# Performance work log

Hardware: AMD Instinct MI355X
Metric: run time of the kernel (lower is better)

The kernel has to match this reference:

```python
import jax, jax.numpy as jnp
import numpy as np

N = 100000   # nodes
E = 1600000  # edges (avg degree 16)
F_IN = 50    # dataset.num_features
C = 32       # dataset.num_classes == hidden == out channels


def setup_inputs() -> dict:
    key = jax.random.key(0)
    ks = jax.random.split(key, 12)
    x = jax.random.normal(ks[0], (N, F_IN), dtype=jnp.float32)
    edge_index = jax.random.randint(ks[1], (2, E), 0, N, dtype=jnp.int64)
    dims = [(F_IN, C), (C, C), (C, C)]
    inp = {"x": x, "edge_index": edge_index}
    for i, (din, dout) in enumerate(dims, start=1):
        s = 1.0 / np.sqrt(din)
        inp[f"Wl{i}"] = jax.random.uniform(ks[2 + 3 * (i - 1)], (din, dout), jnp.float32, -s, s)
        inp[f"bl{i}"] = jax.random.uniform(ks[3 + 3 * (i - 1)], (dout,), jnp.float32, -s, s)
        inp[f"Wr{i}"] = jax.random.uniform(ks[4 + 3 * (i - 1)], (din, dout), jnp.float32, -s, s)
    return inp


def _sage_conv(x, src, dst, Wl, bl, Wr):
    # message = x[src]; scatter-max into dst; lin_l(agg) + lin_r(x)
    msg = x[src]                                      # [E, d_in]
    agg = jax.ops.segment_max(msg, dst, num_segments=N)
    agg = jnp.where(jnp.isfinite(agg), agg, jnp.zeros((), agg.dtype))  # empty segments -> 0
    return agg @ Wl + bl + x @ Wr


def reference(x, edge_index, Wl1, bl1, Wr1, Wl2, bl2, Wr2, Wl3, bl3, Wr3):
    src, dst = edge_index[0], edge_index[1]
    h = jax.nn.relu(_sage_conv(x, src, dst, Wl1, bl1, Wr1))
    h = jax.nn.relu(_sage_conv(h, src, dst, Wl2, bl2, Wr2))
    h = _sage_conv(h, src, dst, Wl3, bl3, Wr3)
    return jax.nn.log_softmax(h, axis=1)
```

## Files before the change

kernel.cpp:

```cpp
#include <hip/hip_runtime.h>
#include <math.h>

#define NN 100000
#define CD 32
#define NPB 4

#define B1N ((NN + 255) >> 8)
#define EPB_A 4096

typedef unsigned int   uint32;
typedef unsigned short ushort16;

__device__ __forceinline__ ushort16 f2b(float f) {
    uint32 u = __float_as_uint(f);
    u = (u + 0x7FFFu + ((u >> 16) & 1u)) >> 16;
    return (ushort16)u;
}
__device__ __forceinline__ float b2f_lo(uint32 u) { return __uint_as_float(u << 16); }
__device__ __forceinline__ float b2f_hi(uint32 u) { return __uint_as_float(u & 0xFFFF0000u); }

__global__ void detect_idx64(const void* edge, int* flag) {
    const long long* p = (const long long*)edge;
    int lane = threadIdx.x & 63;
    int bad = 0;
    for (int i = lane; i < 512; i += 64) {
        long long v = p[i];
        if (v < 0 || v >= NN) bad = 1;
    }
    unsigned long long anybad = __ballot(bad);
    if (lane == 0) *flag = (anybad == 0ULL) ? 1 : 0;
}

__device__ __forceinline__ int load_idx(const void* edge, int i, int is64) {
    if (is64) return (int)((const long long*)edge)[i];
    return ((const int*)edge)[i];
}

__global__ void cvt_x_kernel(const float* __restrict__ x, uint32* __restrict__ xb) {
    const int t = blockIdx.x * blockDim.x + threadIdx.x;
    if (t >= NN * 32) return;
    const int n = t >> 5;
    const int c = t & 31;
    if (c >= 25) { xb[t] = 0; return; }
    float2 v = *(const float2*)&x[n * 50 + 2 * c];
    xb[t] = (uint32)f2b(v.x) | ((uint32)f2b(v.y) << 16);
}


__global__ __launch_bounds__(256) void hist_kernel(const void* edge, int E,
                                                   const int* flag,
                                                   int* __restrict__ hist) {
    __shared__ int lh[B1N];
    const int is64 = *flag;
    const int t = threadIdx.x;
    for (int b = t; b < B1N; b += 256) lh[b] = 0;
    __syncthreads();
    const int e0 = blockIdx.x * EPB_A + t;
#pragma unroll
    for (int k = 0; k < 16; ++k) {
        int e = e0 + k * 256;
        if (e < E) {
            int d = load_idx(edge, E + e, is64);
            atomicAdd(&lh[d >> 8], 1);
        }
    }
    __syncthreads();
    int* gh = hist + (size_t)blockIdx.x * B1N;
    for (int b = t; b < B1N; b += 256) gh[b] = lh[b];
}

__global__ __launch_bounds__(256) void scanA_kernel(int* __restrict__ hist,
                                                    int nblk,
                                                    int* __restrict__ binTotal) {
    __shared__ int ts[256];
    const int bin = blockIdx.x;
    const int t = threadIdx.x;
    const int base = t * 4;
    int v0 = (base + 0 < nblk) ? hist[(size_t)(base + 0) * B1N + bin] : 0;
    int v1 = (base + 1 < nblk) ? hist[(size_t)(base + 1) * B1N + bin] : 0;
    int v2 = (base + 2 < nblk) ? hist[(size_t)(base + 2) * B1N + bin] : 0;
    int v3 = (base + 3 < nblk) ? hist[(size_t)(base + 3) * B1N + bin] : 0;
    const int s = v0 + v1 + v2 + v3;
    ts[t] = s;
    __syncthreads();
    for (int off = 1; off < 256; off <<= 1) {
        int u = (t >= off) ? ts[t - off] : 0;
        __syncthreads();
        ts[t] += u;
        __syncthreads();
    }
    int e = ts[t] - s;
    if (base + 0 < nblk) { hist[(size_t)(base + 0) * B1N + bin] = e; e += v0; }
    if (base + 1 < nblk) { hist[(size_t)(base + 1) * B1N + bin] = e; e += v1; }
    if (base + 2 < nblk) { hist[(size_t)(base + 2) * B1N + bin] = e; e += v2; }
    if (base + 3 < nblk) { hist[(size_t)(base + 3) * B1N + bin] = e; e += v3; }
    if (t == 255) binTotal[bin] = ts[255];
}

__global__ __launch_bounds__(256) void scanB_kernel(const int* __restrict__ binTotal,
                                                    int* __restrict__ binBase) {
    __shared__ int ts[256];
    const int t = threadIdx.x;
    const int base = t * 2;
    const int v0 = (base + 0 < B1N) ? binTotal[base + 0] : 0;
    const int v1 = (base + 1 < B1N) ? binTotal[base + 1] : 0;
    const int s = v0 + v1;
    ts[t] = s;
    __syncthreads();
    for (int off = 1; off < 256; off <<= 1) {
        int u = (t >= off) ? ts[t - off] : 0;
        __syncthreads();
        ts[t] += u;
        __syncthreads();
    }
    const int e = ts[t] - s;
    if (base + 0 < B1N) binBase[base + 0] = e;
    if (base + 1 < B1N) binBase[base + 1] = e + v0;
    if (t == 255) binBase[B1N] = ts[255];
}

__global__ __launch_bounds__(256) void scatter_kernel(const void* edge, int E,
                                                      const int* flag,
                                                      const int* __restrict__ hist,
                                                      const int* __restrict__ binBase,
                                                      uint32* __restrict__ bucketed) {
    __shared__ int cur[B1N];
    const int is64 = *flag;
    const int t = threadIdx.x;
    const int* gh = hist + (size_t)blockIdx.x * B1N;
    for (int b = t; b < B1N; b += 256) cur[b] = binBase[b] + gh[b];
    __syncthreads();
    const int e0 = blockIdx.x * EPB_A + t;
#pragma unroll
    for (int k = 0; k < 16; ++k) {
        int e = e0 + k * 256;
        if (e < E) {
            int s = load_idx(edge, e, is64);
            int d = load_idx(edge, E + e, is64);
            int pos = atomicAdd(&cur[d >> 8], 1);
            bucketed[pos] = (uint32)s | ((uint32)(d & 255) << 17);
        }
    }
}

__global__ __launch_bounds__(256) void bucket_kernel(const uint32* __restrict__ bucketed,
                                                     const int* __restrict__ binBase,
                                                     int* __restrict__ offsets,
                                                     int* __restrict__ csr_src) {
    __shared__ int h[256];
    __shared__ int sc[256];
    __shared__ int cur[256];
    const int bkt = blockIdx.x;
    const int t = threadIdx.x;
    const int start = binBase[bkt];
    const int end   = binBase[bkt + 1];
    h[t] = 0;
    __syncthreads();
    for (int i = start + t; i < end; i += 256)
        atomicAdd(&h[bucketed[i] >> 17], 1);
    __syncthreads();
    const int v = h[t];
    sc[t] = v;
    __syncthreads();
    for (int off = 1; off < 256; off <<= 1) {
        int u = (t >= off) ? sc[t - off] : 0;
        __syncthreads();
        sc[t] += u;
        __syncthreads();
    }
    const int excl = sc[t] - v;
    const int node = bkt * 256 + t;
    if (node < NN) offsets[node] = start + excl;
    cur[t] = start + excl;
    __syncthreads();
    for (int i = start + t; i < end; i += 256) {
        uint32 p = bucketed[i];
        int pos = atomicAdd(&cur[p >> 17], 1);
        csr_src[pos] = (int)(p & 0x1FFFFu);
    }
    if (bkt == B1N - 1 && t == 0) offsets[NN] = end;
}

__global__ void gather50_kernel(const uint32* __restrict__ hb,
                                const int* __restrict__ offsets,
                                const int* __restrict__ csr_src,
                                uint32* __restrict__ aggB) {
    const int tid  = threadIdx.x;
    const int g    = tid >> 6;
    const int lane = tid & 63;
    const int p    = lane >> 5;
    const int j    = lane & 31;
    const int n    = blockIdx.x * NPB + g;
    if (n >= NN) return;

    const float NEG = -INFINITY;
    const int beg = offsets[n];
    const int end = offsets[n + 1];
    const char* hbase = (const char*)hb;
    const uint32 joff = (uint32)(j << 2);

    float lo_[8], hi_[8];
#pragma unroll
    for (int k = 0; k < 8; ++k) { lo_[k] = NEG; hi_[k] = NEG; }
    int i = beg + p;
    for (; i + 14 < end; i += 16) {
        int s[8];
#pragma unroll
        for (int k = 0; k < 8; ++k) s[k] = csr_src[i + 2 * k];
#pragma unroll
        for (int k = 0; k < 8; ++k) {
            uint32 u = *(const uint32*)(hbase + ((((uint32)s[k]) << 7) | joff));
            lo_[k] = fmaxf(lo_[k], b2f_lo(u));
            hi_[k] = fmaxf(hi_[k], b2f_hi(u));
        }
    }
#pragma unroll
    for (int k = 0; k < 7; ++k) {
        if (i + 2 * k < end) {
            uint32 u = *(const uint32*)(hbase + ((((uint32)csr_src[i + 2 * k]) << 7) | joff));
            lo_[k] = fmaxf(lo_[k], b2f_lo(u));
            hi_[k] = fmaxf(hi_[k], b2f_hi(u));
        }
    }
#pragma unroll
    for (int off2 = 4; off2 > 0; off2 >>= 1)
#pragma unroll
        for (int k = 0; k < off2; ++k) {
            lo_[k] = fmaxf(lo_[k], lo_[k + off2]);
            hi_[k] = fmaxf(hi_[k], hi_[k + off2]);
        }
    float lo = lo_[0], hi = hi_[0];
    lo = fmaxf(lo, __shfl_xor(lo, 32));
    hi = fmaxf(hi, __shfl_xor(hi, 32));
    lo = (lo == NEG) ? 0.0f : lo;
    hi = (hi == NEG) ? 0.0f : hi;
    if (p == 0 && j < 25) {
        aggB[(size_t)n * 32 + j] =
            (__float_as_uint(lo) >> 16) | (__float_as_uint(hi) & 0xFFFF0000u);
    }
}

__global__ void gather32_kernel(const uint32* __restrict__ hb,
                                const int* __restrict__ offsets,
                                const int* __restrict__ csr_src,
                                uint32* __restrict__ aggB) {
    const int tid  = threadIdx.x;
    const int g    = tid >> 6;
    const int lane = tid & 63;
    const int e    = lane >> 4;
    const int c    = lane & 15;
    const int n    = blockIdx.x * NPB + g;
    if (n >= NN) return;

    const float NEG = -INFINITY;
    const int beg = offsets[n];
    const int end = offsets[n + 1];
    const char* hbase = (const char*)hb;
    const uint32 coff = (uint32)(c << 2);

    float l0 = NEG, h0 = NEG, l1 = NEG, h1 = NEG;
    float l2 = NEG, h2 = NEG, l3 = NEG, h3 = NEG;
    int i = beg + e;
    for (; i + 12 < end; i += 16) {
        int s0 = csr_src[i];
        int s1 = csr_src[i + 4];
        int s2 = csr_src[i + 8];
        int s3 = csr_src[i + 12];
        uint32 u0 = *(const uint32*)(hbase + ((((uint32)s0) << 6) | coff));
        uint32 u1 = *(const uint32*)(hbase + ((((uint32)s1) << 6) | coff));
        uint32 u2 = *(const uint32*)(hbase + ((((uint32)s2) << 6) | coff));
        uint32 u3 = *(const uint32*)(hbase + ((((uint32)s3) << 6) | coff));
        l0 = fmaxf(l0, b2f_lo(u0)); h0 = fmaxf(h0, b2f_hi(u0));
        l1 = fmaxf(l1, b2f_lo(u1)); h1 = fmaxf(h1, b2f_hi(u1));
        l2 = fmaxf(l2, b2f_lo(u2)); h2 = fmaxf(h2, b2f_hi(u2));
        l3 = fmaxf(l3, b2f_lo(u3)); h3 = fmaxf(h3, b2f_hi(u3));
    }
    if (i < end) {
        uint32 u = *(const uint32*)(hbase + ((((uint32)csr_src[i]) << 6) | coff));
        l0 = fmaxf(l0, b2f_lo(u)); h0 = fmaxf(h0, b2f_hi(u));
    }
    if (i + 4 < end) {
        uint32 u = *(const uint32*)(hbase + ((((uint32)csr_src[i + 4]) << 6) | coff));
        l1 = fmaxf(l1, b2f_lo(u)); h1 = fmaxf(h1, b2f_hi(u));
    }
    if (i + 8 < end) {
        uint32 u = *(const uint32*)(hbase + ((((uint32)csr_src[i + 8]) << 6) | coff));
        l2 = fmaxf(l2, b2f_lo(u)); h2 = fmaxf(h2, b2f_hi(u));
    }
    float lo = fmaxf(fmaxf(l0, l1), fmaxf(l2, l3));
    float hi = fmaxf(fmaxf(h0, h1), fmaxf(h2, h3));
    lo = fmaxf(lo, __shfl_xor(lo, 16));
    hi = fmaxf(hi, __shfl_xor(hi, 16));
    lo = fmaxf(lo, __shfl_xor(lo, 32));
    hi = fmaxf(hi, __shfl_xor(hi, 32));
    lo = (lo == NEG) ? 0.0f : lo;
    hi = (hi == NEG) ? 0.0f : hi;
    if (lane < 16) {
        aggB[(size_t)n * 16 + lane] =
            (__float_as_uint(lo) >> 16) | (__float_as_uint(hi) & 0xFFFF0000u);
    }
}

template <int DIN, int ASTR, int HSTR, int OSTR, int MODE>
__global__ void dense_kernel(const uint32* __restrict__ aggB,
                             const uint32* __restrict__ hB,
                             const float* __restrict__ Wl,
                             const float* __restrict__ bl,
                             const float* __restrict__ Wr,
                             void* __restrict__ out_v) {
    const int n = blockIdx.x * blockDim.x + threadIdx.x;
    if (n >= NN) return;

    float acc[CD];
#pragma unroll
    for (int j = 0; j < CD; ++j) acc[j] = bl[j];

    {
        const uint32* row = aggB + (size_t)n * ASTR;
        for (int c = 0; c < DIN / 4; ++c) {
            uint2 u = *(const uint2*)&row[c * 2];
            float d0 = b2f_lo(u.x), d1 = b2f_hi(u.x);
            float d2 = b2f_lo(u.y), d3 = b2f_hi(u.y);
            const float* w = Wl + c * 4 * CD;
#pragma unroll
            for (int j = 0; j < CD; ++j)
                acc[j] += d0 * w[j] + d1 * w[CD + j] + d2 * w[2 * CD + j] + d3 * w[3 * CD + j];
        }
        if (DIN % 4) {
            uint32 u = row[(DIN / 4) * 2];
            float d0 = b2f_lo(u), d1 = b2f_hi(u);
            const float* w = Wl + (DIN - 2) * CD;
#pragma unroll
            for (int j = 0; j < CD; ++j)
                acc[j] += d0 * w[j] + d1 * w[CD + j];
        }
    }
    {
        const uint32* row = hB + (size_t)n * HSTR;
        for (int c = 0; c < DIN / 4; ++c) {
            uint2 u = *(const uint2*)&row[c * 2];
            float d0 = b2f_lo(u.x), d1 = b2f_hi(u.x);
            float d2 = b2f_lo(u.y), d3 = b2f_hi(u.y);
            const float* w = Wr + c * 4 * CD;
#pragma unroll
            for (int j = 0; j < CD; ++j)
                acc[j] += d0 * w[j] + d1 * w[CD + j] + d2 * w[2 * CD + j] + d3 * w[3 * CD + j];
        }
        if (DIN % 4) {
            uint32 u = row[(DIN / 4) * 2];
            float d0 = b2f_lo(u), d1 = b2f_hi(u);
            const float* w = Wr + (DIN - 2) * CD;
#pragma unroll
            for (int j = 0; j < CD; ++j)
                acc[j] += d0 * w[j] + d1 * w[CD + j];
        }
    }

    if (MODE == 0) {
        uint32* orow = (uint32*)out_v + (size_t)n * OSTR;
#pragma unroll
        for (int c = 0; c < CD / 2; ++c) {
            float a0 = fmaxf(acc[2 * c],     0.0f);
            float a1 = fmaxf(acc[2 * c + 1], 0.0f);
            orow[c] = (uint32)f2b(a0) | ((uint32)f2b(a1) << 16);
        }
    } else {
        float m = acc[0];
#pragma unroll
        for (int j = 1; j < CD; ++j) m = fmaxf(m, acc[j]);
        float s = 0.0f;
#pragma unroll
        for (int j = 0; j < CD; ++j) s += expf(acc[j] - m);
        const float lse = m + logf(s);
        float* orow = (float*)out_v + (size_t)n * CD;
#pragma unroll
        for (int j = 0; j < CD; ++j) orow[j] = acc[j] - lse;
    }
}

extern "C" void kernel_launch(void* const* d_in, const int* in_sizes, int n_in,
                              void* d_out, int out_size, void* d_ws, size_t ws_size,
                              hipStream_t stream) {
    const float* x    = (const float*)d_in[0];
    const void*  edge = d_in[1];
    const float* Wl1 = (const float*)d_in[2];
    const float* bl1 = (const float*)d_in[3];
    const float* Wr1 = (const float*)d_in[4];
    const float* Wl2 = (const float*)d_in[5];
    const float* bl2 = (const float*)d_in[6];
    const float* Wr2 = (const float*)d_in[7];
    const float* Wl3 = (const float*)d_in[8];
    const float* bl3 = (const float*)d_in[9];
    const float* Wr3 = (const float*)d_in[10];

    const int E = in_sizes[1] / 2;

    char* ws = (char*)d_ws;
    size_t off = 0;
    auto carve = [&](size_t bytes) {
        void* p = ws + off;
        off = (off + bytes + 255) & ~(size_t)255;
        return p;
    };
    int*    offsets   = (int*)   carve((size_t)(NN + 1) * 4);
    int*    flag      = (int*)   carve(4);
    int*    binTotal  = (int*)   carve((size_t)B1N * 4);
    int*    binBase   = (int*)   carve((size_t)(B1N + 1) * 4);
    int*    csr_src   = (int*)   carve((size_t)E * 4);
    uint32* xb        = (uint32*)carve((size_t)NN * 32 * 4);
    uint32* h1b       = (uint32*)carve((size_t)NN * 16 * 4);
    (void)ws_size; (void)n_in; (void)out_size;

    uint32* bucketed = (uint32*)d_out;
    int*    hist     = (int*)((char*)d_out + (((size_t)E * 4 + 255) & ~(size_t)255));
    uint32* agg1 = (uint32*)d_out;
    uint32* agg2 = (uint32*)d_out;
    uint32* h2b  = xb;
    uint32* agg3 = h1b;

    detect_idx64<<<1, 64, 0, stream>>>(edge, flag);
    cvt_x_kernel<<<(NN * 32 + 255) / 256, 256, 0, stream>>>(x, xb);

    const int nblkA = (E + EPB_A - 1) / EPB_A;
    hist_kernel<<<nblkA, 256, 0, stream>>>(edge, E, flag, hist);
    scanA_kernel<<<B1N, 256, 0, stream>>>(hist, nblkA, binTotal);
    scanB_kernel<<<1, 256, 0, stream>>>(binTotal, binBase);
    scatter_kernel<<<nblkA, 256, 0, stream>>>(edge, E, flag, hist, binBase, bucketed);
    bucket_kernel<<<B1N, 256, 0, stream>>>(bucketed, binBase, offsets, csr_src);

    const int gb = (NN + NPB - 1) / NPB;
    const int db = (NN + 255) / 256;

    gather50_kernel<<<gb, 256, 0, stream>>>(xb, offsets, csr_src, agg1);
    dense_kernel<50, 32, 32, 16, 0><<<db, 256, 0, stream>>>(agg1, xb, Wl1, bl1, Wr1, h1b);
    gather32_kernel<<<gb, 256, 0, stream>>>(h1b, offsets, csr_src, agg2);
    dense_kernel<32, 16, 16, 16, 0><<<db, 256, 0, stream>>>(agg2, h1b, Wl2, bl2, Wr2, h2b);
    gather32_kernel<<<gb, 256, 0, stream>>>(h2b, offsets, csr_src, agg3);
    dense_kernel<32, 16, 16, 0, 2><<<db, 256, 0, stream>>>(agg3, h2b, Wl3, bl3, Wr3, d_out);
}
```

Before: 344.0 us.

## Fuse gather and dense phases per layer; inline index-width detect and bin scan

Merges each layer's neighbor max-gather with its dense projection into one kernel. The aggregate and self features stay in LDS and each wavefront computes the 32 outputs with lanes split across the Wl and Wr halves, so the bf16 aggregate no longer round-trips through global memory. The index-width detection kernel and the single-block bin-base scan are folded into their consumer kernels, where every block recomputes them redundantly, and edges per block are halved. This removes several launches and intermediate buffers, at the cost of per-lane serial dot products reading weights from global or cache and repeated small scans in each block.

After: 342.1 us. No clear change (-0.6%).

```diff
diff --git a/kernel.cpp b/kernel.cpp
--- a/kernel.cpp
+++ b/kernel.cpp
@@ -6,7 +6,7 @@
 #define NPB 4
 
 #define B1N ((NN + 255) >> 8)
-#define EPB_A 4096
+#define EPB_A 2048
 
 typedef unsigned int   uint32;
 typedef unsigned short ushort16;
@@ -19,7 +19,7 @@
 __device__ __forceinline__ float b2f_lo(uint32 u) { return __uint_as_float(u << 16); }
 __device__ __forceinline__ float b2f_hi(uint32 u) { return __uint_as_float(u & 0xFFFF0000u); }
 
-__global__ void detect_idx64(const void* edge, int* flag) {
+__device__ __forceinline__ int edge_is64(const void* edge) {
     const long long* p = (const long long*)edge;
     int lane = threadIdx.x & 63;
     int bad = 0;
@@ -28,7 +28,7 @@
         if (v < 0 || v >= NN) bad = 1;
     }
     unsigned long long anybad = __ballot(bad);
-    if (lane == 0) *flag = (anybad == 0ULL) ? 1 : 0;
+    return (anybad == 0ULL) ? 1 : 0;
 }
 
 __device__ __forceinline__ int load_idx(const void* edge, int i, int is64) {
@@ -48,16 +48,15 @@
 
 
 __global__ __launch_bounds__(256) void hist_kernel(const void* edge, int E,
-                                                   const int* flag,
                                                    int* __restrict__ hist) {
     __shared__ int lh[B1N];
-    const int is64 = *flag;
+    const int is64 = edge_is64(edge);
     const int t = threadIdx.x;
     for (int b = t; b < B1N; b += 256) lh[b] = 0;
     __syncthreads();
     const int e0 = blockIdx.x * EPB_A + t;
 #pragma unroll
-    for (int k = 0; k < 16; ++k) {
+    for (int k = 0; k < 8; ++k) {
         int e = e0 + k * 256;
         if (e < E) {
             int d = load_idx(edge, E + e, is64);
@@ -97,9 +96,8 @@
     if (t == 255) binTotal[bin] = ts[255];
 }
 
-__global__ __launch_bounds__(256) void scanB_kernel(const int* __restrict__ binTotal,
-                                                    int* __restrict__ binBase) {
-    __shared__ int ts[256];
+__device__ __forceinline__ void scan_bins_lds(const int* __restrict__ binTotal,
+                                              int* ts, int* lbase) {
     const int t = threadIdx.x;
     const int base = t * 2;
     const int v0 = (base + 0 < B1N) ? binTotal[base + 0] : 0;
@@ -114,25 +112,28 @@
         __syncthreads();
     }
     const int e = ts[t] - s;
-    if (base + 0 < B1N) binBase[base + 0] = e;
-    if (base + 1 < B1N) binBase[base + 1] = e + v0;
-    if (t == 255) binBase[B1N] = ts[255];
+    if (base + 0 < B1N) lbase[base + 0] = e;
+    if (base + 1 < B1N) lbase[base + 1] = e + v0;
+    if (t == 255) lbase[B1N] = ts[255];
+    __syncthreads();
 }
 
 __global__ __launch_bounds__(256) void scatter_kernel(const void* edge, int E,
-                                                      const int* flag,
                                                       const int* __restrict__ hist,
-                                                      const int* __restrict__ binBase,
+                                                      const int* __restrict__ binTotal,
                                                       uint32* __restrict__ bucketed) {
+    __shared__ int ts[256];
+    __shared__ int lbase[B1N + 1];
     __shared__ int cur[B1N];
-    const int is64 = *flag;
+    const int is64 = edge_is64(edge);
     const int t = threadIdx.x;
+    scan_bins_lds(binTotal, ts, lbase);
     const int* gh = hist + (size_t)blockIdx.x * B1N;
-    for (int b = t; b < B1N; b += 256) cur[b] = binBase[b] + gh[b];
+    for (int b = t; b < B1N; b += 256) cur[b] = lbase[b] + gh[b];
     __syncthreads();
     const int e0 = blockIdx.x * EPB_A + t;
 #pragma unroll
-    for (int k = 0; k < 16; ++k) {
+    for (int k = 0; k < 8; ++k) {
         int e = e0 + k * 256;
         if (e < E) {
             int s = load_idx(edge, e, is64);
@@ -144,16 +145,19 @@
 }
 
 __global__ __launch_bounds__(256) void bucket_kernel(const uint32* __restrict__ bucketed,
-                                                     const int* __restrict__ binBase,
+                                                     const int* __restrict__ binTotal,
                                                      int* __restrict__ offsets,
                                                      int* __restrict__ csr_src) {
+    __shared__ int ts[256];
+    __shared__ int lbase[B1N + 1];
     __shared__ int h[256];
     __shared__ int sc[256];
     __shared__ int cur[256];
     const int bkt = blockIdx.x;
     const int t = threadIdx.x;
-    const int start = binBase[bkt];
-    const int end   = binBase[bkt + 1];
+    scan_bins_lds(binTotal, ts, lbase);
+    const int start = lbase[bkt];
+    const int end   = lbase[bkt + 1];
     h[t] = 0;
     __syncthreads();
     for (int i = start + t; i < end; i += 256)
@@ -181,10 +185,52 @@
     if (bkt == B1N - 1 && t == 0) offsets[NN] = end;
 }
 
-__global__ void gather50_kernel(const uint32* __restrict__ hb,
-                                const int* __restrict__ offsets,
-                                const int* __restrict__ csr_src,
-                                uint32* __restrict__ aggB) {
+
+template <int DIN, int MODE>
+__device__ __forceinline__ void dense_phase(const float* lds_agg, const float* lds_x,
+                                            const float* __restrict__ Wl,
+                                            const float* __restrict__ bl,
+                                            const float* __restrict__ Wr,
+                                            int n, void* __restrict__ out_v, int lane) {
+    const int l = lane & 31;
+    const int p = lane >> 5;
+    const float* W   = p ? Wr : Wl;
+    const float* src = p ? lds_x : lds_agg;
+    float acc = 0.0f;
+#pragma unroll
+    for (int c = 0; c < DIN; ++c)
+        acc += src[c] * W[c * CD + l];
+    acc += __shfl_xor(acc, 32);
+    acc += bl[l];
+    if (MODE == 0) {
+        float r = fmaxf(acc, 0.0f);
+        float a = __shfl(r, 2 * l);
+        float b = __shfl(r, 2 * l + 1);
+        if (lane < 16) {
+            ((uint32*)out_v)[(size_t)n * 16 + lane] =
+                (uint32)f2b(a) | ((uint32)f2b(b) << 16);
+        }
+    } else {
+        float m = acc;
+#pragma unroll
+        for (int o = 1; o < 32; o <<= 1) m = fmaxf(m, __shfl_xor(m, o));
+        float e = expf(acc - m);
+        float s = e;
+#pragma unroll
+        for (int o = 1; o < 32; o <<= 1) s += __shfl_xor(s, o);
+        const float lse = m + logf(s);
+        if (p == 0) ((float*)out_v)[(size_t)n * CD + l] = acc - lse;
+    }
+}
+
+__global__ void fused50_kernel(const uint32* __restrict__ hb,
+                               const int* __restrict__ offsets,
+                               const int* __restrict__ csr_src,
+                               const float* __restrict__ Wl,
+                               const float* __restrict__ bl,
+                               const float* __restrict__ Wr,
+                               void* __restrict__ out_v) {
+    __shared__ float lds_buf[NPB][2][64];
     const int tid  = threadIdx.x;
     const int g    = tid >> 6;
     const int lane = tid & 63;
@@ -193,11 +239,20 @@
     const int n    = blockIdx.x * NPB + g;
     if (n >= NN) return;
 
+    float* lds_agg = lds_buf[g][0];
+    float* lds_x   = lds_buf[g][1];
+
     const float NEG = -INFINITY;
     const int beg = offsets[n];
     const int end = offsets[n + 1];
     const char* hbase = (const char*)hb;
     const uint32 joff = (uint32)(j << 2);
+
+    if (p == 1 && j < 25) {
+        uint32 u = hb[(size_t)n * 32 + j];
+        lds_x[2 * j]     = b2f_lo(u);
+        lds_x[2 * j + 1] = b2f_hi(u);
+    }
 
     float lo_[8], hi_[8];
 #pragma unroll
@@ -235,15 +290,21 @@
     lo = (lo == NEG) ? 0.0f : lo;
     hi = (hi == NEG) ? 0.0f : hi;
     if (p == 0 && j < 25) {
-        aggB[(size_t)n * 32 + j] =
-            (__float_as_uint(lo) >> 16) | (__float_as_uint(hi) & 0xFFFF0000u);
-    }
-}
-
-__global__ void gather32_kernel(const uint32* __restrict__ hb,
-                                const int* __restrict__ offsets,
-                                const int* __restrict__ csr_src,
-                                uint32* __restrict__ aggB) {
+        lds_agg[2 * j]     = lo;
+        lds_agg[2 * j + 1] = hi;
+    }
+    dense_phase<50, 0>(lds_agg, lds_x, Wl, bl, Wr, n, out_v, lane);
+}
+
+template <int MODE>
+__global__ void fused32_kernel(const uint32* __restrict__ hb,
+                               const int* __restrict__ offsets,
+                               const int* __restrict__ csr_src,
+                               const float* __restrict__ Wl,
+                               const float* __restrict__ bl,
+                               const float* __restrict__ Wr,
+                               void* __restrict__ out_v) {
+    __shared__ float lds_buf[NPB][2][64];
     const int tid  = threadIdx.x;
     const int g    = tid >> 6;
     const int lane = tid & 63;
@@ -252,11 +313,20 @@
     const int n    = blockIdx.x * NPB + g;
     if (n >= NN) return;
 
+    float* lds_agg = lds_buf[g][0];
+    float* lds_x   = lds_buf[g][1];
+
     const float NEG = -INFINITY;
     const int beg = offsets[n];
     const int end = offsets[n + 1];
     const char* hbase = (const char*)hb;
     const uint32 coff = (uint32)(c << 2);
+
+    if (e == 1) {
+        uint32 u = hb[(size_t)n * 16 + c];
+        lds_x[2 * c]     = b2f_lo(u);
+        lds_x[2 * c + 1] = b2f_hi(u);
+    }
 
     float l0 = NEG, h0 = NEG, l1 = NEG, h1 = NEG;
     float l2 = NEG, h2 = NEG, l3 = NEG, h3 = NEG;
@@ -296,86 +366,10 @@
     lo = (lo == NEG) ? 0.0f : lo;
     hi = (hi == NEG) ? 0.0f : hi;
     if (lane < 16) {
-        aggB[(size_t)n * 16 + lane] =
-            (__float_as_uint(lo) >> 16) | (__float_as_uint(hi) & 0xFFFF0000u);
-    }
-}
-
-template <int DIN, int ASTR, int HSTR, int OSTR, int MODE>
-__global__ void dense_kernel(const uint32* __restrict__ aggB,
-                             const uint32* __restrict__ hB,
-                             const float* __restrict__ Wl,
-                             const float* __restrict__ bl,
-                             const float* __restrict__ Wr,
-                             void* __restrict__ out_v) {
-    const int n = blockIdx.x * blockDim.x + threadIdx.x;
-    if (n >= NN) return;
-
-    float acc[CD];
-#pragma unroll
-    for (int j = 0; j < CD; ++j) acc[j] = bl[j];
-
-    {
-        const uint32* row = aggB + (size_t)n * ASTR;
-        for (int c = 0; c < DIN / 4; ++c) {
-            uint2 u = *(const uint2*)&row[c * 2];
-            float d0 = b2f_lo(u.x), d1 = b2f_hi(u.x);
-            float d2 = b2f_lo(u.y), d3 = b2f_hi(u.y);
-            const float* w = Wl + c * 4 * CD;
-#pragma unroll
-            for (int j = 0; j < CD; ++j)
-                acc[j] += d0 * w[j] + d1 * w[CD + j] + d2 * w[2 * CD + j] + d3 * w[3 * CD + j];
-        }
-        if (DIN % 4) {
-            uint32 u = row[(DIN / 4) * 2];
-            float d0 = b2f_lo(u), d1 = b2f_hi(u);
-            const float* w = Wl + (DIN - 2) * CD;
-#pragma unroll
-            for (int j = 0; j < CD; ++j)
-                acc[j] += d0 * w[j] + d1 * w[CD + j];
-        }
-    }
-    {
-        const uint32* row = hB + (size_t)n * HSTR;
-        for (int c = 0; c < DIN / 4; ++c) {
-            uint2 u = *(const uint2*)&row[c * 2];
-            float d0 = b2f_lo(u.x), d1 = b2f_hi(u.x);
-            float d2 = b2f_lo(u.y), d3 = b2f_hi(u.y);
-            const float* w = Wr + c * 4 * CD;
-#pragma unroll
-            for (int j = 0; j < CD; ++j)
-                acc[j] += d0 * w[j] + d1 * w[CD + j] + d2 * w[2 * CD + j] + d3 * w[3 * CD + j];
-        }
-        if (DIN % 4) {
-            uint32 u = row[(DIN / 4) * 2];
-            float d0 = b2f_lo(u), d1 = b2f_hi(u);
-            const float* w = Wr + (DIN - 2) * CD;
-#pragma unroll
-            for (int j = 0; j < CD; ++j)
-                acc[j] += d0 * w[j] + d1 * w[CD + j];
-        }
-    }
-
-    if (MODE == 0) {
-        uint32* orow = (uint32*)out_v + (size_t)n * OSTR;
-#pragma unroll
-        for (int c = 0; c < CD / 2; ++c) {
-            float a0 = fmaxf(acc[2 * c],     0.0f);
-            float a1 = fmaxf(acc[2 * c + 1], 0.0f);
-            orow[c] = (uint32)f2b(a0) | ((uint32)f2b(a1) << 16);
-        }
-    } else {
-        float m = acc[0];
-#pragma unroll
-        for (int j = 1; j < CD; ++j) m = fmaxf(m, acc[j]);
-        float s = 0.0f;
-#pragma unroll
-        for (int j = 0; j < CD; ++j) s += expf(acc[j] - m);
-        const float lse = m + logf(s);
-        float* orow = (float*)out_v + (size_t)n * CD;
-#pragma unroll
-        for (int j = 0; j < CD; ++j) orow[j] = acc[j] - lse;
-    }
+        lds_agg[2 * c]     = lo;
+        lds_agg[2 * c + 1] = hi;
+    }
+    dense_phase<32, MODE>(lds_agg, lds_x, Wl, bl, Wr, n, out_v, lane);
 }
 
 extern "C" void kernel_launch(void* const* d_in, const int* in_sizes, int n_in,
@@ -403,9 +397,7 @@
         return p;
     };
     int*    offsets   = (int*)   carve((size_t)(NN + 1) * 4);
-    int*    flag      = (int*)   carve(4);
     int*    binTotal  = (int*)   carve((size_t)B1N * 4);
-    int*    binBase   = (int*)   carve((size_t)(B1N + 1) * 4);
     int*    csr_src   = (int*)   carve((size_t)E * 4);
     uint32* xb        = (uint32*)carve((size_t)NN * 32 * 4);
     uint32* h1b       = (uint32*)carve((size_t)NN * 16 * 4);
@@ -413,28 +405,19 @@
 
     uint32* bucketed = (uint32*)d_out;
     int*    hist     = (int*)((char*)d_out + (((size_t)E * 4 + 255) & ~(size_t)255));
-    uint32* agg1 = (uint32*)d_out;
-    uint32* agg2 = (uint32*)d_out;
     uint32* h2b  = xb;
-    uint32* agg3 = h1b;
-
-    detect_idx64<<<1, 64, 0, stream>>>(edge, flag);
+
     cvt_x_kernel<<<(NN * 32 + 255) / 256, 256, 0, stream>>>(x, xb);
 
     const int nblkA = (E + EPB_A - 1) / EPB_A;
-    hist_kernel<<<nblkA, 256, 0, stream>>>(edge, E, flag, hist);
+    hist_kernel<<<nblkA, 256, 0, stream>>>(edge, E, hist);
     scanA_kernel<<<B1N, 256, 0, stream>>>(hist, nblkA, binTotal);
-    scanB_kernel<<<1, 256, 0, stream>>>(binTotal, binBase);
-    scatter_kernel<<<nblkA, 256, 0, stream>>>(edge, E, flag, hist, binBase, bucketed);
-    bucket_kernel<<<B1N, 256, 0, stream>>>(bucketed, binBase, offsets, csr_src);
+    scatter_kernel<<<nblkA, 256, 0, stream>>>(edge, E, hist, binTotal, bucketed);
+    bucket_kernel<<<B1N, 256, 0, stream>>>(bucketed, binTotal, offsets, csr_src);
 
     const int gb = (NN + NPB - 1) / NPB;
-    const int db = (NN + 255) / 256;
-
-    gather50_kernel<<<gb, 256, 0, stream>>>(xb, offsets, csr_src, agg1);
-    dense_kernel<50, 32, 32, 16, 0><<<db, 256, 0, stream>>>(agg1, xb, Wl1, bl1, Wr1, h1b);
-    gather32_kernel<<<gb, 256, 0, stream>>>(h1b, offsets, csr_src, agg2);
-    dense_kernel<32, 16, 16, 16, 0><<<db, 256, 0, stream>>>(agg2, h1b, Wl2, bl2, Wr2, h2b);
-    gather32_kernel<<<gb, 256, 0, stream>>>(h2b, offsets, csr_src, agg3);
-    dense_kernel<32, 16, 16, 0, 2><<<db, 256, 0, stream>>>(agg3, h2b, Wl3, bl3, Wr3, d_out);
-}
+
+    fused50_kernel<<<gb, 256, 0, stream>>>(xb, offsets, csr_src, Wl1, bl1, Wr1, h1b);
+    fused32_kernel<0><<<gb, 256, 0, stream>>>(h1b, offsets, csr_src, Wl2, bl2, Wr2, h2b);
+    fused32_kernel<2><<<gb, 256, 0, stream>>>(h2b, offsets, csr_src, Wl3, bl3, Wr3, d_out);
+}
```

## Fold index-width detection and bin scan into consumers; shuffle-broadcast CSR indices in gathers

Applied to the files above, without the earlier changes.

The separate detect_idx64 and scanB kernel launches are removed. Each hist, scatter and bucket block now recomputes the 64-bit index check and the small bin-offset scan in LDS, trading a little redundant work per block for two fewer launches and serialized dependencies. The gather kernels now load a chunk of 64 CSR source indices once per wave with a coalesced read and hand them out with __shfl, instead of every lane re-reading the same indices from memory. EPB_A is halved so the histogram and scatter passes run on twice as many blocks.

New measurement: 316.2 us. -8.1%, faster.

```diff
diff --git a/kernel.cpp b/kernel.cpp
--- a/kernel.cpp
+++ b/kernel.cpp
@@ -6,7 +6,7 @@
 #define NPB 4
 
 #define B1N ((NN + 255) >> 8)
-#define EPB_A 4096
+#define EPB_A 2048
 
 typedef unsigned int   uint32;
 typedef unsigned short ushort16;
@@ -19,7 +19,7 @@
 __device__ __forceinline__ float b2f_lo(uint32 u) { return __uint_as_float(u << 16); }
 __device__ __forceinline__ float b2f_hi(uint32 u) { return __uint_as_float(u & 0xFFFF0000u); }
 
-__global__ void detect_idx64(const void* edge, int* flag) {
+__device__ __forceinline__ int edge_is64(const void* edge) {
     const long long* p = (const long long*)edge;
     int lane = threadIdx.x & 63;
     int bad = 0;
@@ -28,7 +28,7 @@
         if (v < 0 || v >= NN) bad = 1;
     }
     unsigned long long anybad = __ballot(bad);
-    if (lane == 0) *flag = (anybad == 0ULL) ? 1 : 0;
+    return (anybad == 0ULL) ? 1 : 0;
 }
 
 __device__ __forceinline__ int load_idx(const void* edge, int i, int is64) {
@@ -48,16 +48,15 @@
 
 
 __global__ __launch_bounds__(256) void hist_kernel(const void* edge, int E,
-                                                   const int* flag,
                                                    int* __restrict__ hist) {
     __shared__ int lh[B1N];
-    const int is64 = *flag;
+    const int is64 = edge_is64(edge);
     const int t = threadIdx.x;
     for (int b = t; b < B1N; b += 256) lh[b] = 0;
     __syncthreads();
     const int e0 = blockIdx.x * EPB_A + t;
 #pragma unroll
-    for (int k = 0; k < 16; ++k) {
+    for (int k = 0; k < 8; ++k) {
         int e = e0 + k * 256;
         if (e < E) {
             int d = load_idx(edge, E + e, is64);
@@ -97,9 +96,8 @@
     if (t == 255) binTotal[bin] = ts[255];
 }
 
-__global__ __launch_bounds__(256) void scanB_kernel(const int* __restrict__ binTotal,
-                                                    int* __restrict__ binBase) {
-    __shared__ int ts[256];
+__device__ __forceinline__ void scan_bins_lds(const int* __restrict__ binTotal,
+                                              int* ts, int* lbase) {
     const int t = threadIdx.x;
     const int base = t * 2;
     const int v0 = (base + 0 < B1N) ? binTotal[base + 0] : 0;
@@ -114,25 +112,28 @@
         __syncthreads();
     }
     const int e = ts[t] - s;
-    if (base + 0 < B1N) binBase[base + 0] = e;
-    if (base + 1 < B1N) binBase[base + 1] = e + v0;
-    if (t == 255) binBase[B1N] = ts[255];
+    if (base + 0 < B1N) lbase[base + 0] = e;
+    if (base + 1 < B1N) lbase[base + 1] = e + v0;
+    if (t == 255) lbase[B1N] = ts[255];
+    __syncthreads();
 }
 
 __global__ __launch_bounds__(256) void scatter_kernel(const void* edge, int E,
-                                                      const int* flag,
                                                       const int* __restrict__ hist,
-                                                      const int* __restrict__ binBase,
+                                                      const int* __restrict__ binTotal,
                                                       uint32* __restrict__ bucketed) {
+    __shared__ int ts[256];
+    __shared__ int lbase[B1N + 1];
     __shared__ int cur[B1N];
-    const int is64 = *flag;
+    const int is64 = edge_is64(edge);
     const int t = threadIdx.x;
+    scan_bins_lds(binTotal, ts, lbase);
     const int* gh = hist + (size_t)blockIdx.x * B1N;
-    for (int b = t; b < B1N; b += 256) cur[b] = binBase[b] + gh[b];
+    for (int b = t; b < B1N; b += 256) cur[b] = lbase[b] + gh[b];
     __syncthreads();
     const int e0 = blockIdx.x * EPB_A + t;
 #pragma unroll
-    for (int k = 0; k < 16; ++k) {
+    for (int k = 0; k < 8; ++k) {
         int e = e0 + k * 256;
         if (e < E) {
             int s = load_idx(edge, e, is64);
@@ -144,16 +145,19 @@
 }
 
 __global__ __launch_bounds__(256) void bucket_kernel(const uint32* __restrict__ bucketed,
-                                                     const int* __restrict__ binBase,
+                                                     const int* __restrict__ binTotal,
                                                      int* __restrict__ offsets,
                                                      int* __restrict__ csr_src) {
+    __shared__ int ts[256];
+    __shared__ int lbase[B1N + 1];
     __shared__ int h[256];
     __shared__ int sc[256];
     __shared__ int cur[256];
     const int bkt = blockIdx.x;
     const int t = threadIdx.x;
-    const int start = binBase[bkt];
-    const int end   = binBase[bkt + 1];
+    scan_bins_lds(binTotal, ts, lbase);
+    const int start = lbase[bkt];
+    const int end   = lbase[bkt + 1];
     h[t] = 0;
     __syncthreads();
     for (int i = start + t; i < end; i += 256)
@@ -180,6 +184,7 @@
     }
     if (bkt == B1N - 1 && t == 0) offsets[NN] = end;
 }
+
 
 __global__ void gather50_kernel(const uint32* __restrict__ hb,
                                 const int* __restrict__ offsets,
@@ -198,28 +203,44 @@
     const int end = offsets[n + 1];
     const char* hbase = (const char*)hb;
     const uint32 joff = (uint32)(j << 2);
+    const int lb = p << 5;
 
     float lo_[8], hi_[8];
 #pragma unroll
     for (int k = 0; k < 8; ++k) { lo_[k] = NEG; hi_[k] = NEG; }
-    int i = beg + p;
-    for (; i + 14 < end; i += 16) {
-        int s[8];
-#pragma unroll
-        for (int k = 0; k < 8; ++k) s[k] = csr_src[i + 2 * k];
-#pragma unroll
-        for (int k = 0; k < 8; ++k) {
-            uint32 u = *(const uint32*)(hbase + ((((uint32)s[k]) << 7) | joff));
-            lo_[k] = fmaxf(lo_[k], b2f_lo(u));
-            hi_[k] = fmaxf(hi_[k], b2f_hi(u));
-        }
-    }
-#pragma unroll
-    for (int k = 0; k < 7; ++k) {
-        if (i + 2 * k < end) {
-            uint32 u = *(const uint32*)(hbase + ((((uint32)csr_src[i + 2 * k]) << 7) | joff));
-            lo_[k] = fmaxf(lo_[k], b2f_lo(u));
-            hi_[k] = fmaxf(hi_[k], b2f_hi(u));
+
+    for (int ib = beg; ib < end; ib += 64) {
+        const int rem = end - ib;
+        const int mm  = rem < 64 ? rem : 64;
+        const int myidx = 2 * j + p;
+        int sidx = 0;
+        if (myidx < mm) sidx = csr_src[ib + myidx];
+        int k = p;
+        for (; k + 14 < mm; k += 16) {
+            const int kh = lb + (k >> 1);
+#pragma unroll
+            for (int kk = 0; kk < 8; ++kk) {
+                int s = __shfl(sidx, kh + kk);
+                uint32 u = *(const uint32*)(hbase + ((((uint32)s) << 7) | joff));
+                lo_[kk] = fmaxf(lo_[kk], b2f_lo(u));
+                hi_[kk] = fmaxf(hi_[kk], b2f_hi(u));
+            }
+        }
+        for (; k + 6 < mm; k += 8) {
+            const int kh = lb + (k >> 1);
+#pragma unroll
+            for (int kk = 0; kk < 4; ++kk) {
+                int s = __shfl(sidx, kh + kk);
+                uint32 u = *(const uint32*)(hbase + ((((uint32)s) << 7) | joff));
+                lo_[kk] = fmaxf(lo_[kk], b2f_lo(u));
+                hi_[kk] = fmaxf(hi_[kk], b2f_hi(u));
+            }
+        }
+        for (; k < mm; k += 2) {
+            int s = __shfl(sidx, lb + (k >> 1));
+            uint32 u = *(const uint32*)(hbase + ((((uint32)s) << 7) | joff));
+            lo_[0] = fmaxf(lo_[0], b2f_lo(u));
+            hi_[0] = fmaxf(hi_[0], b2f_hi(u));
         }
     }
 #pragma unroll
@@ -257,35 +278,38 @@
     const int end = offsets[n + 1];
     const char* hbase = (const char*)hb;
     const uint32 coff = (uint32)(c << 2);
+    const int lb = e << 4;
 
     float l0 = NEG, h0 = NEG, l1 = NEG, h1 = NEG;
     float l2 = NEG, h2 = NEG, l3 = NEG, h3 = NEG;
-    int i = beg + e;
-    for (; i + 12 < end; i += 16) {
-        int s0 = csr_src[i];
-        int s1 = csr_src[i + 4];
-        int s2 = csr_src[i + 8];
-        int s3 = csr_src[i + 12];
-        uint32 u0 = *(const uint32*)(hbase + ((((uint32)s0) << 6) | coff));
-        uint32 u1 = *(const uint32*)(hbase + ((((uint32)s1) << 6) | coff));
-        uint32 u2 = *(const uint32*)(hbase + ((((uint32)s2) << 6) | coff));
-        uint32 u3 = *(const uint32*)(hbase + ((((uint32)s3) << 6) | coff));
-        l0 = fmaxf(l0, b2f_lo(u0)); h0 = fmaxf(h0, b2f_hi(u0));
-        l1 = fmaxf(l1, b2f_lo(u1)); h1 = fmaxf(h1, b2f_hi(u1));
-        l2 = fmaxf(l2, b2f_lo(u2)); h2 = fmaxf(h2, b2f_hi(u2));
-        l3 = fmaxf(l3, b2f_lo(u3)); h3 = fmaxf(h3, b2f_hi(u3));
-    }
-    if (i < end) {
-        uint32 u = *(const uint32*)(hbase + ((((uint32)csr_src[i]) << 6) | coff));
-        l0 = fmaxf(l0, b2f_lo(u)); h0 = fmaxf(h0, b2f_hi(u));
-    }
-    if (i + 4 < end) {
-        uint32 u = *(const uint32*)(hbase + ((((uint32)csr_src[i + 4]) << 6) | coff));
-        l1 = fmaxf(l1, b2f_lo(u)); h1 = fmaxf(h1, b2f_hi(u));
-    }
-    if (i + 8 < end) {
-        uint32 u = *(const uint32*)(hbase + ((((uint32)csr_src[i + 8]) << 6) | coff));
-        l2 = fmaxf(l2, b2f_lo(u)); h2 = fmaxf(h2, b2f_hi(u));
+
+    for (int ib = beg; ib < end; ib += 64) {
+        const int rem = end - ib;
+        const int mm  = rem < 64 ? rem : 64;
+        const int myidx = 4 * c + e;
+        int sidx = 0;
+        if (myidx < mm) sidx = csr_src[ib + myidx];
+        int k = e;
+        for (; k + 12 < mm; k += 16) {
+            const int m = lb + (k >> 2);
+            int s0 = __shfl(sidx, m);
+            int s1 = __shfl(sidx, m + 1);
+            int s2 = __shfl(sidx, m + 2);
+            int s3 = __shfl(sidx, m + 3);
+            uint32 u0 = *(const uint32*)(hbase + ((((uint32)s0) << 6) | coff));
+            uint32 u1 = *(const uint32*)(hbase + ((((uint32)s1) << 6) | coff));
+            uint32 u2 = *(const uint32*)(hbase + ((((uint32)s2) << 6) | coff));
+            uint32 u3 = *(const uint32*)(hbase + ((((uint32)s3) << 6) | coff));
+            l0 = fmaxf(l0, b2f_lo(u0)); h0 = fmaxf(h0, b2f_hi(u0));
+            l1 = fmaxf(l1, b2f_lo(u1)); h1 = fmaxf(h1, b2f_hi(u1));
+            l2 = fmaxf(l2, b2f_lo(u2)); h2 = fmaxf(h2, b2f_hi(u2));
+            l3 = fmaxf(l3, b2f_lo(u3)); h3 = fmaxf(h3, b2f_hi(u3));
+        }
+        for (; k < mm; k += 4) {
+            int s = __shfl(sidx, lb + (k >> 2));
+            uint32 u = *(const uint32*)(hbase + ((((uint32)s) << 6) | coff));
+            l0 = fmaxf(l0, b2f_lo(u)); h0 = fmaxf(h0, b2f_hi(u));
+        }
     }
     float lo = fmaxf(fmaxf(l0, l1), fmaxf(l2, l3));
     float hi = fmaxf(fmaxf(h0, h1), fmaxf(h2, h3));
@@ -403,9 +427,7 @@
         return p;
     };
     int*    offsets   = (int*)   carve((size_t)(NN + 1) * 4);
-    int*    flag      = (int*)   carve(4);
     int*    binTotal  = (int*)   carve((size_t)B1N * 4);
-    int*    binBase   = (int*)   carve((size_t)(B1N + 1) * 4);
     int*    csr_src   = (int*)   carve((size_t)E * 4);
     uint32* xb        = (uint32*)carve((size_t)NN * 32 * 4);
     uint32* h1b       = (uint32*)carve((size_t)NN * 16 * 4);
@@ -418,15 +440,13 @@
     uint32* h2b  = xb;
     uint32* agg3 = h1b;
 
-    detect_idx64<<<1, 64, 0, stream>>>(edge, flag);
     cvt_x_kernel<<<(NN * 32 + 255) / 256, 256, 0, stream>>>(x, xb);
 
     const int nblkA = (E + EPB_A - 1) / EPB_A;
-    hist_kernel<<<nblkA, 256, 0, stream>>>(edge, E, flag, hist);
+    hist_kernel<<<nblkA, 256, 0, stream>>>(edge, E, hist);
     scanA_kernel<<<B1N, 256, 0, stream>>>(hist, nblkA, binTotal);
-    scanB_kernel<<<1, 256, 0, stream>>>(binTotal, binBase);
-    scatter_kernel<<<nblkA, 256, 0, stream>>>(edge, E, flag, hist, binBase, bucketed);
-    bucket_kernel<<<B1N, 256, 0, stream>>>(bucketed, binBase, offsets, csr_src);
+    scatter_kernel<<<nblkA, 256, 0, stream>>>(edge, E, hist, binTotal, bucketed);
+    bucket_kernel<<<B1N, 256, 0, stream>>>(bucketed, binTotal, offsets, csr_src);
 
     const int gb = (NN + NPB - 1) / NPB;
     const int db = (NN + 255) / 256;
```
